# Optimization experiments

Measured on AMD Instinct MI355X. Metric: run time of the kernel, lower is better.

Reference implementation:

```python
import jax, jax.numpy as jnp
import numpy as np

B, D, K, NDIM = 4, 81, 2048, 4  # batch, feature dim, n mixture components, box coord dims


def setup_inputs() -> dict:
    key = jax.random.key(0)
    k1, k2, k3, k4 = jax.random.split(key, 4)
    x = jax.random.normal(k1, (B, D, K), dtype=jnp.float32)
    # mixture weights, positive and normalized over components
    pi = jax.nn.softmax(jax.random.normal(k2, (B, 1, K), dtype=jnp.float32), axis=2)
    # component means in [0,1] (normalized box coords)
    mu = jax.random.uniform(k3, (B, NDIM, K), dtype=jnp.float32)
    # positive scales
    sig = jax.random.uniform(k4, (B, NDIM, K), dtype=jnp.float32) * 0.1 + 0.01
    return {"x": x, "pi": pi, "mu": mu, "sig": sig}


def _cauchy_pdf(mu, sig, points):
    # mu, sig: (B, 1, NDIM, K); points: (B, P, NDIM, 1)
    d = points - mu
    return sig / (jnp.pi * (d * d + sig * sig))


def reference(x, pi, mu, sig):
    # points = mu.transpose(1,2): evaluate the mixture at each component mean
    points = jnp.transpose(mu, (0, 2, 1))            # (B, K, NDIM)
    comp = _cauchy_pdf(mu[:, None, :, :], sig[:, None, :, :],
                       points[:, :, :, None])        # (B, K, NDIM, K)
    comp = jnp.prod(comp, axis=2)                    # independent dims -> (B, K, K)
    lh = pi * comp                                   # pi (B,1,K) broadcasts over points
    coef = lh / jnp.sum(lh, axis=2, keepdims=True)   # normalize over components
    coef = jax.lax.stop_gradient(coef)               # coef_detach=True
    y = jnp.einsum('bdk,bkm->bdm', x, coef)          # torch.bmm(x, coef)
    return y
```

## Files before the change

### kernel.cpp

```cpp
#include <hip/hip_runtime.h>


typedef float v4f __attribute__((ext_vector_type(4)));
typedef float f32x4 __attribute__((ext_vector_type(4)));
typedef short bf16x8 __attribute__((ext_vector_type(8)));

namespace {
constexpr int BB = 4;
constexpr int DD = 81;
constexpr int KK = 2048;
constexpr int MROWS = 96;
constexpr float INV_PI4 = 1.0f / 97.40909103400243f;

constexpr size_t OFF_LHT = 0;
constexpr size_t OFF_XBF = (size_t)BB * KK * KK * 2;
constexpr size_t OFF_RSP = OFF_XBF + (size_t)BB * MROWS * KK * 2;
}

__device__ __forceinline__ unsigned short f2bf(float f) {
    union { float f; unsigned int u; } v; v.f = f;
    unsigned int u = v.u;
    unsigned int r = (u + 0x7FFFu + ((u >> 16) & 1u)) >> 16;
    return (unsigned short)r;
}

__global__ __launch_bounds__(256) void prep1_kernel(const float* __restrict__ pi_,
                                                    const float* __restrict__ mu,
                                                    const float* __restrict__ sig,
                                                    unsigned short* __restrict__ lhT,
                                                    float* __restrict__ rowsumPart) {
    __shared__ v4f   mush[256];
    __shared__ v4f   s2sh[256];
    __shared__ float csh[256];
    __shared__ float red[4][64];

    int blk = blockIdx.x;
    int b   = blk >> 8;
    int pc  = (blk & 255) >> 3;
    int ms  = blk & 7;
    int p0  = pc * 64;
    int m0  = ms * 256;
    int t   = threadIdx.x;
    int lane = t & 63, w = t >> 6;

    const float* mub = mu  + (size_t)b * 4 * KK;
    const float* sgb = sig + (size_t)b * 4 * KK;
    const float* pib = pi_ + (size_t)b * KK;

    {
        int m = m0 + t;
        v4f mm = {mub[m], mub[KK + m], mub[2 * KK + m], mub[3 * KK + m]};
        v4f sg = {sgb[m], sgb[KK + m], sgb[2 * KK + m], sgb[3 * KK + m]};
        mush[t] = mm;
        s2sh[t] = sg * sg;
        csh[t]  = pib[m] * ((sg.x * sg.y) * (sg.z * sg.w)) * INV_PI4;
    }
    int p = p0 + lane;
    v4f mp = {mub[p], mub[KK + p], mub[2 * KK + p], mub[3 * KK + p]};
    __syncthreads();

    unsigned short* lbase = lhT + (size_t)b * KK * KK + p0 + lane;
    float sum = 0.f;
#pragma unroll 4
    for (int i = 0; i < 64; ++i) {
        int mi = w * 64 + i;
        v4f d = mp - mush[mi];
        v4f q = d * d + s2sh[mi];
        float den = (q.x * q.y) * (q.z * q.w);
        float lh = csh[mi] * __builtin_amdgcn_rcpf(den);
        sum += lh;
        lbase[(size_t)(m0 + mi) * KK] = f2bf(lh);
    }

    red[w][lane] = sum;
    __syncthreads();
    if (t < 64)
        rowsumPart[((size_t)(b * 8 + ms)) * KK + p0 + t] =
            red[0][t] + red[1][t] + red[2][t] + red[3][t];
}

__global__ __launch_bounds__(256) void xbf_kernel(const float* __restrict__ x,
                                                  const float* __restrict__ rowsumPart,
                                                  unsigned short* __restrict__ xbf) {
    int d = blockIdx.x;
    int b = blockIdx.y;
    int t = threadIdx.x;
    unsigned short* orow = xbf + ((size_t)(b * MROWS + d)) * KK;
    const float* xrow = x + ((size_t)(b * DD + d)) * KK;
    const float* rsp  = rowsumPart + (size_t)b * 8 * KK;
#pragma unroll
    for (int j = 0; j < 8; ++j) {
        int p = j * 256 + t;
        float rs = 0.f;
#pragma unroll
        for (int s = 0; s < 8; ++s) rs += rsp[(size_t)s * KK + p];
        float v = 0.f;
        if (d < DD) v = xrow[p] * __builtin_amdgcn_rcpf(rs);
        orow[p] = f2bf(v);
    }
}

__global__ __launch_bounds__(512) void gemm_kernel(const unsigned short* __restrict__ xbf,
                                                   const unsigned short* __restrict__ lhT,
                                                   float* __restrict__ out) {
    __shared__ f32x4 lds[8][6][64];

    int t = threadIdx.x;
    int w = t >> 6, lane = t & 63;
    int r = lane & 15, q = lane >> 4;

    int b  = blockIdx.y;
    int m0 = blockIdx.x * 16;
    int p0 = w * 256;

    const unsigned short* Abase = xbf + ((size_t)(b * MROWS + r)) * KK;
    const unsigned short* Bbase = lhT + ((size_t)(b * KK + m0 + r)) * KK;

    f32x4 acc[6];
#pragma unroll
    for (int i = 0; i < 6; ++i) acc[i] = (f32x4)0.f;

#pragma unroll 4
    for (int ks = 0; ks < 8; ++ks) {
        int p = p0 + ks * 32 + q * 8;
        bf16x8 Bf = *(const bf16x8*)(Bbase + p);
        bf16x8 Af[6];
#pragma unroll
        for (int Mt = 0; Mt < 6; ++Mt)
            Af[Mt] = *(const bf16x8*)(Abase + (size_t)Mt * 16 * KK + p);
#pragma unroll
        for (int Mt = 0; Mt < 6; ++Mt)
            acc[Mt] = __builtin_amdgcn_mfma_f32_16x16x32_bf16(Af[Mt], Bf, acc[Mt], 0, 0, 0);
    }

#pragma unroll
    for (int Mt = 0; Mt < 6; ++Mt)
        lds[w][Mt][lane] = acc[Mt];
    __syncthreads();

    int col = t & 15;
    int dr  = t >> 4;
#pragma unroll
    for (int k = 0; k < 3; ++k) {
        int d = dr + 32 * k;
        if (d < DD) {
            int Mt  = d >> 4;
            int row = d & 15;
            int l   = (row >> 2) * 16 + col;
            int j   = row & 3;
            float s = 0.f;
#pragma unroll
            for (int ww = 0; ww < 8; ++ww) s += lds[ww][Mt][l][j];
            out[((size_t)(b * DD + d)) * KK + m0 + col] = s;
        }
    }
}

extern "C" void kernel_launch(void* const* d_in, const int* in_sizes, int n_in,
                              void* d_out, int out_size, void* d_ws, size_t ws_size,
                              hipStream_t stream) {
    const float* x   = (const float*)d_in[0];
    const float* pi_ = (const float*)d_in[1];
    const float* mu  = (const float*)d_in[2];
    const float* sig = (const float*)d_in[3];
    float* out = (float*)d_out;

    unsigned short* lhT = (unsigned short*)((char*)d_ws + OFF_LHT);
    unsigned short* xbf = (unsigned short*)((char*)d_ws + OFF_XBF);
    float* rowsumPart   = (float*)((char*)d_ws + OFF_RSP);

    prep1_kernel<<<1024, 256, 0, stream>>>(pi_, mu, sig, lhT, rowsumPart);
    dim3 xg(MROWS, BB);
    xbf_kernel<<<xg, 256, 0, stream>>>(x, rowsumPart, xbf);
    dim3 gg(KK / 16, BB);
    gemm_kernel<<<gg, 512, 0, stream>>>(xbf, lhT, out);
}
```

Baseline: 109.5 us.

## Recompute Cauchy likelihood matrix inside GEMM instead of materializing it

The prep kernel no longer writes the B*K*K bf16 likelihood matrix; it only computes row sums. The GEMM kernel stages the component means in LDS and recomputes each likelihood entry on the fly to build the MFMA B operand. This drops roughly 32 MB of global write and read traffic in exchange for the likelihood arithmetic being done twice (once for the row sums, once in the GEMM) and more ALU work per MFMA. LDS use also grows to 48KB per block.

```diff
diff --git a/kernel.cpp b/kernel.cpp
--- a/kernel.cpp
+++ b/kernel.cpp
@@ -12,9 +12,8 @@
 constexpr int MROWS = 96;
 constexpr float INV_PI4 = 1.0f / 97.40909103400243f;
 
-constexpr size_t OFF_LHT = 0;
-constexpr size_t OFF_XBF = (size_t)BB * KK * KK * 2;
-constexpr size_t OFF_RSP = OFF_XBF + (size_t)BB * MROWS * KK * 2;
+constexpr size_t OFF_XBF = 0;
+constexpr size_t OFF_RSP = (size_t)BB * MROWS * KK * 2;
 }
 
 __device__ __forceinline__ unsigned short f2bf(float f) {
@@ -24,11 +23,10 @@
     return (unsigned short)r;
 }
 
-__global__ __launch_bounds__(256) void prep1_kernel(const float* __restrict__ pi_,
-                                                    const float* __restrict__ mu,
-                                                    const float* __restrict__ sig,
-                                                    unsigned short* __restrict__ lhT,
-                                                    float* __restrict__ rowsumPart) {
+__global__ __launch_bounds__(256) void rowsum_kernel(const float* __restrict__ pi_,
+                                                     const float* __restrict__ mu,
+                                                     const float* __restrict__ sig,
+                                                     float* __restrict__ rowsumPart) {
     __shared__ v4f   mush[256];
     __shared__ v4f   s2sh[256];
     __shared__ float csh[256];
@@ -59,7 +57,6 @@
     v4f mp = {mub[p], mub[KK + p], mub[2 * KK + p], mub[3 * KK + p]};
     __syncthreads();
 
-    unsigned short* lbase = lhT + (size_t)b * KK * KK + p0 + lane;
     float sum = 0.f;
 #pragma unroll 4
     for (int i = 0; i < 64; ++i) {
@@ -67,9 +64,7 @@
         v4f d = mp - mush[mi];
         v4f q = d * d + s2sh[mi];
         float den = (q.x * q.y) * (q.z * q.w);
-        float lh = csh[mi] * __builtin_amdgcn_rcpf(den);
-        sum += lh;
-        lbase[(size_t)(m0 + mi) * KK] = f2bf(lh);
+        sum += csh[mi] * __builtin_amdgcn_rcpf(den);
     }
 
     red[w][lane] = sum;
@@ -100,42 +95,68 @@
     }
 }
 
-__global__ __launch_bounds__(512) void gemm_kernel(const unsigned short* __restrict__ xbf,
-                                                   const unsigned short* __restrict__ lhT,
+__global__ __launch_bounds__(512) void gemm_kernel(const float* __restrict__ pi_,
+                                                   const float* __restrict__ mu,
+                                                   const float* __restrict__ sig,
+                                                   const unsigned short* __restrict__ xbf,
                                                    float* __restrict__ out) {
-    __shared__ f32x4 lds[8][6][64];
+    __shared__ __align__(16) char smem[49152];
+    v4f* mus = (v4f*)smem;
+    f32x4 (*red)[6][64] = (f32x4 (*)[6][64])smem;
 
     int t = threadIdx.x;
     int w = t >> 6, lane = t & 63;
     int r = lane & 15, q = lane >> 4;
-
     int b  = blockIdx.y;
     int m0 = blockIdx.x * 16;
-    int p0 = w * 256;
+
+    const float* mub = mu  + (size_t)b * 4 * KK;
+    const float* sgb = sig + (size_t)b * 4 * KK;
+
+    for (int i = t; i < KK; i += 512)
+        mus[i] = (v4f){mub[i], mub[KK + i], mub[2 * KK + i], mub[3 * KK + i]};
+
+    int m = m0 + r;
+    v4f mm = {mub[m], mub[KK + m], mub[2 * KK + m], mub[3 * KK + m]};
+    v4f sg = {sgb[m], sgb[KK + m], sgb[2 * KK + m], sgb[3 * KK + m]};
+    v4f s2 = sg * sg;
+    float cm = pi_[(size_t)b * KK + m] * ((sg.x * sg.y) * (sg.z * sg.w)) * INV_PI4;
 
     const unsigned short* Abase = xbf + ((size_t)(b * MROWS + r)) * KK;
-    const unsigned short* Bbase = lhT + ((size_t)(b * KK + m0 + r)) * KK;
 
     f32x4 acc[6];
 #pragma unroll
     for (int i = 0; i < 6; ++i) acc[i] = (f32x4)0.f;
 
-#pragma unroll 4
+    __syncthreads();
+
+    int pw = w * 256;
+#pragma unroll
     for (int ks = 0; ks < 8; ++ks) {
-        int p = p0 + ks * 32 + q * 8;
-        bf16x8 Bf = *(const bf16x8*)(Bbase + p);
+        int pb = pw + ks * 32 + q * 8;
+        bf16x8 Bf;
+#pragma unroll
+        for (int j = 0; j < 8; ++j) {
+            v4f mp = mus[pb + j];
+            v4f dd = mp - mm;
+            v4f qq = dd * dd + s2;
+            float den = (qq.x * qq.y) * (qq.z * qq.w);
+            float lh = cm * __builtin_amdgcn_rcpf(den);
+            Bf[j] = (short)f2bf(lh);
+        }
         bf16x8 Af[6];
 #pragma unroll
         for (int Mt = 0; Mt < 6; ++Mt)
-            Af[Mt] = *(const bf16x8*)(Abase + (size_t)Mt * 16 * KK + p);
+            Af[Mt] = *(const bf16x8*)(Abase + (size_t)Mt * 16 * KK + pb);
 #pragma unroll
         for (int Mt = 0; Mt < 6; ++Mt)
             acc[Mt] = __builtin_amdgcn_mfma_f32_16x16x32_bf16(Af[Mt], Bf, acc[Mt], 0, 0, 0);
     }
 
+    __syncthreads();
 #pragma unroll
     for (int Mt = 0; Mt < 6; ++Mt)
-        lds[w][Mt][lane] = acc[Mt];
+        red[w][Mt][lane] = acc[Mt];
     __syncthreads();
 
     int col = t & 15;
@@ -150,7 +171,7 @@
             int j   = row & 3;
             float s = 0.f;
 #pragma unroll
-            for (int ww = 0; ww < 8; ++ww) s += lds[ww][Mt][l][j];
+            for (int ww = 0; ww < 8; ++ww) s += red[ww][Mt][l][j];
             out[((size_t)(b * DD + d)) * KK + m0 + col] = s;
         }
     }
@@ -165,13 +186,12 @@
     const float* sig = (const float*)d_in[3];
     float* out = (float*)d_out;
 
-    unsigned short* lhT = (unsigned short*)((char*)d_ws + OFF_LHT);
     unsigned short* xbf = (unsigned short*)((char*)d_ws + OFF_XBF);
     float* rowsumPart   = (float*)((char*)d_ws + OFF_RSP);
 
-    prep1_kernel<<<1024, 256, 0, stream>>>(pi_, mu, sig, lhT, rowsumPart);
+    rowsum_kernel<<<1024, 256, 0, stream>>>(pi_, mu, sig, rowsumPart);
     dim3 xg(MROWS, BB);
     xbf_kernel<<<xg, 256, 0, stream>>>(x, rowsumPart, xbf);
     dim3 gg(KK / 16, BB);
-    gemm_kernel<<<gg, 512, 0, stream>>>(xbf, lhT, out);
+    gemm_kernel<<<gg, 512, 0, stream>>>(pi_, mu, sig, xbf, out);
 }
```

New measurement: 100.2 us. 1.09x faster.
